# Performance work log

Hardware: AMD Instinct MI355X
Metric: run time of the kernel (lower is better)

## Reference

```python
import jax, jax.numpy as jnp
import numpy as np

B, S, DIN, D = 8, 1024, 512, 512


def _xavier(key, fan_in, fan_out):
    bound = float(np.sqrt(6.0 / (fan_in + fan_out)))
    return jax.random.uniform(key, (fan_in, fan_out), jnp.float32, -bound, bound)


def setup_inputs() -> dict:
    key = jax.random.key(0)
    ks = jax.random.split(key, 6)
    return {
        'x': jax.random.normal(ks[0], (B, S, DIN), jnp.float32),
        # weights stored as [in, out] (transpose of torch Linear.weight); biases zero-init per _init_weights
        'W_in': _xavier(ks[1], DIN, 4 * D), 'b_in': jnp.zeros((4 * D,), jnp.float32),
        'W_ig': _xavier(ks[2], D, D), 'b_ig': jnp.zeros((D,), jnp.float32),
        'W_fg': _xavier(ks[3], D, D), 'b_fg': jnp.zeros((D,), jnp.float32),
        'W_og': _xavier(ks[4], D, D), 'b_og': jnp.zeros((D,), jnp.float32),
        'W_out': _xavier(ks[5], D, D), 'b_out': jnp.zeros((D,), jnp.float32),
    }


def reference(x, W_in, b_in, W_ig, b_ig, W_fg, b_fg, W_og, b_og, W_out, b_out):
    b, s, _ = x.shape
    d = W_ig.shape[0]
    proj = x @ W_in + b_in                      # [B,S,4D]
    q, k, v, _g = jnp.split(proj, 4, axis=-1)   # g (silu branch) is unused in the original loop
    q = jnp.tanh(q)
    k = jnp.tanh(k)
    # dropout is identity in eval mode
    i_g = jax.nn.sigmoid(v @ W_ig + b_ig)       # per-step gates are pointwise linears -> batch them
    f_g = jax.nn.sigmoid(v @ W_fg + b_fg)
    o_g = jax.nn.sigmoid(v @ W_og + b_og)

    def step(carry, ts):
        C, n = carry                            # C: [B,D,D], n: [B,D]
        qt, kt, vt, it, ft, ot = ts             # each [B,D]
        C = ft[:, :, None] * C + it[:, :, None] * (kt[:, :, None] * vt[:, None, :])
        n = ft * n + it * kt
        h_cand = jnp.einsum('bd,bde->be', qt, C)
        denom = jnp.maximum(jnp.sum(qt * n, axis=-1, keepdims=True), 1e-6)
        h = ot * h_cand / denom
        return (C, n), h

    tm = lambda a: jnp.swapaxes(a, 0, 1)        # time-major for scan
    C0 = jnp.zeros((b, d, d), x.dtype)
    n0 = jnp.zeros((b, d), x.dtype)
    (Cf, nf), hs = jax.lax.scan(step, (C0, n0), (tm(q), tm(k), tm(v), tm(i_g), tm(f_g), tm(o_g)))
    hs = jnp.swapaxes(hs, 0, 1)                 # [B,S,D]
    out = hs @ W_out + b_out
    return out, Cf, nf, hs[:, -1, :]
```

## Files before the change

kernel.cpp:

```cpp
#include <hip/hip_runtime.h>

#define S_ 1024
#define D_ 512
#define DCH 4
#define NDCH 256
#define CT 32
#define NCT 32

using bf16x8 = __attribute__((ext_vector_type(8))) short;
using f32x4  = __attribute__((ext_vector_type(4))) float;

__device__ __forceinline__ unsigned short f2bf(float x) {
    unsigned int u = __float_as_uint(x);
    u = (u + 0x7FFFu + ((u >> 16) & 1u)) >> 16;
    return (unsigned short)u;
}
__device__ __forceinline__ float bf2f(unsigned short s) {
    return __uint_as_float(((unsigned int)s) << 16);
}
__device__ __forceinline__ bf16x8 cvt8(const float* __restrict__ p) {
    float4 a = *(const float4*)p;
    float4 b = *(const float4*)(p + 4);
    bf16x8 r;
    r[0] = (short)f2bf(a.x); r[1] = (short)f2bf(a.y);
    r[2] = (short)f2bf(a.z); r[3] = (short)f2bf(a.w);
    r[4] = (short)f2bf(b.x); r[5] = (short)f2bf(b.y);
    r[6] = (short)f2bf(b.z); r[7] = (short)f2bf(b.w);
    return r;
}
__device__ __forceinline__ void gload_lds16(const void* g, void* l) {
    __builtin_amdgcn_global_load_lds(
        (const __attribute__((address_space(1))) void*)g,
        (__attribute__((address_space(3))) void*)l, 16, 0, 0);
}


__global__ __launch_bounds__(256)
void prep_w(const float* __restrict__ W_in, const float* __restrict__ W_ig,
            const float* __restrict__ W_fg, const float* __restrict__ W_og,
            const float* __restrict__ W_out,
            unsigned short* __restrict__ Wh, unsigned short* __restrict__ Wl)
{
    const int n    = blockIdx.x * 256 + threadIdx.x;
    const int kblk = blockIdx.y;

    const float* src; int ldw, col;
    if (n < 1536)       { src = W_in;  ldw = 2048; col = n; }
    else if (n < 3072)  {
        const int g = (n - 1536) >> 9;
        src = (g == 0) ? W_ig : (g == 1) ? W_fg : W_og;
        ldw = 512; col = (n - 1536) & 511;
    } else              { src = W_out; ldw = 512; col = n - 3072; }

    unsigned int hw[16], lw[16];
#pragma unroll
    for (int j = 0; j < 32; j += 2) {
        const int k = kblk * 32 + j;
        float f0 = src[(size_t)k * ldw + col];
        float f1 = src[(size_t)(k + 1) * ldw + col];
        unsigned short h0 = f2bf(f0), h1 = f2bf(f1);
        unsigned short l0 = f2bf(f0 - bf2f(h0)), l1 = f2bf(f1 - bf2f(h1));
        hw[j >> 1] = (unsigned int)h0 | ((unsigned int)h1 << 16);
        lw[j >> 1] = (unsigned int)l0 | ((unsigned int)l1 << 16);
    }
    const size_t base = ((size_t)(n >> 7) * 16 + kblk) * 4096 + ((n & 127) << 5);
    const int perm = (n >> 1) & 3;
#pragma unroll
    for (int g = 0; g < 4; ++g) {
        const size_t dst = base + (size_t)((g ^ perm) << 3);
        *(uint4*)(Wh + dst) = make_uint4(hw[g*4], hw[g*4+1], hw[g*4+2], hw[g*4+3]);
        *(uint4*)(Wl + dst) = make_uint4(lw[g*4], lw[g*4+1], lw[g*4+2], lw[g*4+3]);
    }
}

__global__ __launch_bounds__(256)
void cvt_a(const float* __restrict__ A, int lda,
           unsigned short* __restrict__ Ah, unsigned short* __restrict__ Al)
{
    const int m    = blockIdx.x * 256 + threadIdx.x;
    const int kblk = blockIdx.y;
    const float* p = A + (size_t)m * lda + kblk * 32;
    const size_t base = ((size_t)(m >> 7) * 16 + kblk) * 4096 + ((m & 127) << 5);
    const int perm = (m >> 1) & 3;
#pragma unroll
    for (int g = 0; g < 4; ++g) {
        float4 a = *(const float4*)(p + g * 8);
        float4 b = *(const float4*)(p + g * 8 + 4);
        float f[8] = {a.x, a.y, a.z, a.w, b.x, b.y, b.z, b.w};
        unsigned int hw[4], lw[4];
#pragma unroll
        for (int j = 0; j < 4; ++j) {
            unsigned short h0 = f2bf(f[2*j]), h1 = f2bf(f[2*j+1]);
            unsigned short l0 = f2bf(f[2*j] - bf2f(h0));
            unsigned short l1 = f2bf(f[2*j+1] - bf2f(h1));
            hw[j] = (unsigned int)h0 | ((unsigned int)h1 << 16);
            lw[j] = (unsigned int)l0 | ((unsigned int)l1 << 16);
        }
        const size_t dst = base + (size_t)((g ^ perm) << 3);
        *(uint4*)(Ah + dst) = make_uint4(hw[0], hw[1], hw[2], hw[3]);
        *(uint4*)(Al + dst) = make_uint4(lw[0], lw[1], lw[2], lw[3]);
    }
}

template<int MODE>
__global__ __launch_bounds__(256)
void gemm_mfma(const unsigned short* __restrict__ Ah,
               const unsigned short* __restrict__ Al,
               const unsigned short* __restrict__ Wh,
               const unsigned short* __restrict__ Wl,
               const float* __restrict__ qkv,
               const float* __restrict__ bb0, const float* __restrict__ bb1,
               const float* __restrict__ bb2,
               float* __restrict__ Co, int ldc,
               unsigned short* __restrict__ Av, unsigned short* __restrict__ Alv)
{
    __shared__ unsigned short lds[2][4][4096];

    const int tid  = threadIdx.x;
    const int lane = tid & 63;
    const int wv   = tid >> 6;
    const int nbt  = (MODE == 2) ? 4 : 12;
    const int cpx  = gridDim.x >> 3;
    const int swz  = (blockIdx.x & 7) * cpx + (blockIdx.x >> 3);
    const int n0blk = swz % nbt;
    const int m0blk = swz / nbt;
    const int l15  = lane & 15;
    const int kg   = lane >> 4;
    const int nbase = (MODE == 0) ? 0 : (MODE == 1) ? 1536 : 3072;

    const size_t abase = (size_t)m0blk * 16 * 4096;
    const size_t wbase = (size_t)((nbase >> 7) + n0blk) * 16 * 4096;

    f32x4 acc[4][4];
#pragma unroll
    for (int mf = 0; mf < 4; ++mf)
#pragma unroll
        for (int nf = 0; nf < 4; ++nf) acc[mf][nf] = (f32x4){0.f, 0.f, 0.f, 0.f};

    auto STAGE = [&](int buf, int kblk) {
        const unsigned short* srcs[4] = {
            Ah + abase + (size_t)kblk * 4096, Al + abase + (size_t)kblk * 4096,
            Wh + wbase + (size_t)kblk * 4096, Wl + wbase + (size_t)kblk * 4096};
#pragma unroll
        for (int p = 0; p < 4; ++p)
#pragma unroll
            for (int h = 0; h < 2; ++h)
                gload_lds16(srcs[p] + h * 2048 + (size_t)tid * 8,
                            &lds[buf][p][h * 2048 + wv * 512]);
    };

    STAGE(0, 0);
    __syncthreads();

    int cur = 0;
    for (int ks = 0; ks < 16; ++ks) {
        if (ks + 1 < 16) STAGE(cur ^ 1, ks + 1);

        bf16x8 ah[4], al[4], bh[4], bl[4];
#pragma unroll
        for (int i = 0; i < 4; ++i) {
            const int ra = (wv >> 1) * 64 + i * 16 + l15;
            const int oa = ra * 32 + ((kg ^ ((ra >> 1) & 3)) << 3);
            ah[i] = *(const bf16x8*)&lds[cur][0][oa];
            al[i] = *(const bf16x8*)&lds[cur][1][oa];
            const int rw = (wv & 1) * 64 + i * 16 + l15;
            const int ow = rw * 32 + ((kg ^ ((rw >> 1) & 3)) << 3);
            bh[i] = *(const bf16x8*)&lds[cur][2][ow];
            bl[i] = *(const bf16x8*)&lds[cur][3][ow];
        }
#pragma unroll
        for (int nf = 0; nf < 4; ++nf)
#pragma unroll
            for (int mf = 0; mf < 4; ++mf) {
                acc[mf][nf] = __builtin_amdgcn_mfma_f32_16x16x32_bf16(ah[mf], bh[nf], acc[mf][nf], 0, 0, 0);
                acc[mf][nf] = __builtin_amdgcn_mfma_f32_16x16x32_bf16(al[mf], bh[nf], acc[mf][nf], 0, 0, 0);
                acc[mf][nf] = __builtin_amdgcn_mfma_f32_16x16x32_bf16(ah[mf], bl[nf], acc[mf][nf], 0, 0, 0);
            }
        __syncthreads();
        cur ^= 1;
    }

    const int m0 = m0blk * 128 + (wv >> 1) * 64;
    const int n0 = n0blk * 128 + (wv & 1) * 64;
#pragma unroll
    for (int mf = 0; mf < 4; ++mf) {
#pragma unroll
        for (int vi = 0; vi < 4; ++vi) {
            const int m = m0 + mf * 16 + kg * 4 + vi;
            float* crow = Co + (size_t)m * ldc;
#pragma unroll
            for (int nf = 0; nf < 4; ++nf) {
                const int n = n0 + nf * 16 + l15;
                float bias;
                if (MODE == 1) {
                    const int g = n >> 9;
                    bias = (g == 0 ? bb0 : g == 1 ? bb1 : bb2)[n & 511];
                } else {
                    bias = bb0[n];
                }
                float v = acc[mf][nf][vi] + bias;
                if (MODE == 0) {
                    if (n < 1024) v = tanhf(v);
                } else if (MODE == 1) {
                    v = 1.0f / (1.0f + expf(-v));
                    if (n < 512) v *= qkv[(size_t)m * 1536 + 512 + n];
                }
                crow[n] = v;
                if (MODE == 0 && Av != nullptr && n >= 1024) {
                    const int k = n - 1024;
                    unsigned short h0 = f2bf(v);
                    unsigned short l0 = f2bf(v - bf2f(h0));
                    const size_t dst = ((size_t)(m >> 7) * 16 + (k >> 5)) * 4096
                                     + ((m & 127) << 5)
                                     + ((((k >> 3) & 3) ^ ((m >> 1) & 3)) << 3)
                                     + (k & 7);
                    Av[dst]  = h0;
                    Alv[dst] = l0;
                }
            }
        }
    }
}

__global__ __launch_bounds__(512)
void nscan_local(const float* __restrict__ GG,
                 double* __restrict__ nend, double* __restrict__ Dend)
{
    const int b = blockIdx.x >> 8;
    const int c = blockIdx.x & 255;
    const int d = threadIdx.x;
    const float* gb = GG + (size_t)b * S_ * 1536 + (size_t)c * DCH * 1536;
    double n = 0.0, P = 1.0;
    for (int u = 0; u < DCH; ++u) {
        const float* row = gb + (size_t)u * 1536;
        const double ik = (double)row[d];
        const double f  = (double)row[512 + d];
        n = fma(f, n, ik);
        P *= f;
    }
    nend[(size_t)blockIdx.x * 512 + d] = n;
    Dend[(size_t)blockIdx.x * 512 + d] = P;
}

__global__ __launch_bounds__(512)
void nscan_stitch(const double* __restrict__ nend, const double* __restrict__ Dend,
                  double* __restrict__ n0a, float* __restrict__ nfO)
{
    const int b = blockIdx.x;
    const int d = threadIdx.x;
    double n0 = 0.0;
    for (int c = 0; c < NDCH; ++c) {
        const size_t idx = ((size_t)(b * NDCH + c)) * 512 + d;
        n0a[idx] = n0;
        n0 = fma(Dend[idx], n0, nend[idx]);
    }
    nfO[(size_t)b * 512 + d] = (float)n0;
}

__global__ __launch_bounds__(256)
void denom_kernel(const float* __restrict__ QKV, const float* __restrict__ GG,
                  const double* __restrict__ n0a, float* __restrict__ invd)
{
    const int lane = threadIdx.x & 63;
    const int widx = blockIdx.x * 4 + (threadIdx.x >> 6);
    const int b    = widx >> 8;
    const int c    = widx & 255;
    const int d0   = 4 * lane;

    const float* qb = QKV + (size_t)b * S_ * 1536 + (size_t)c * DCH * 1536;
    const float* gb = GG  + (size_t)b * S_ * 1536 + (size_t)c * DCH * 1536;
    const double* sp = n0a + (size_t)widx * 512;

    double n[2][4];
#pragma unroll
    for (int r = 0; r < 2; ++r) {
        double2 a = *(const double2*)(sp + d0 + 256 * r);
        double2 bb = *(const double2*)(sp + d0 + 256 * r + 2);
        n[r][0] = a.x; n[r][1] = a.y; n[r][2] = bb.x; n[r][3] = bb.y;
    }

    for (int t0 = 0; t0 < DCH; t0 += 4) {
        double dq[4];
#pragma unroll
        for (int i = 0; i < 4; ++i) {
            const float* qr = qb + (size_t)(t0 + i) * 1536;
            const float* gr = gb + (size_t)(t0 + i) * 1536;
            double acc = 0.0;
#pragma unroll
            for (int r = 0; r < 2; ++r) {
                float4 qf = *(const float4*)(qr + d0 + 256 * r);
                float4 kf = *(const float4*)(gr + d0 + 256 * r);
                float4 ff = *(const float4*)(gr + 512 + d0 + 256 * r);
                const float* qp = (const float*)&qf;
                const float* kp = (const float*)&kf;
                const float* fp = (const float*)&ff;
#pragma unroll
                for (int j = 0; j < 4; ++j) {
                    n[r][j] = fma((double)fp[j], n[r][j], (double)kp[j]);
                    acc = fma((double)qp[j], n[r][j], acc);
                }
            }
            dq[i] = acc;
        }
        double u0 = dq[0] + __shfl_xor(dq[0], 32);
        double u1 = dq[1] + __shfl_xor(dq[1], 32);
        double u2 = dq[2] + __shfl_xor(dq[2], 32);
        double u3 = dq[3] + __shfl_xor(dq[3], 32);
        double w0 = (lane & 32) ? u2 : u0;
        double w1 = (lane & 32) ? u3 : u1;
        w0 += __shfl_xor(w0, 16);
        w1 += __shfl_xor(w1, 16);
        double y = (lane & 16) ? w1 : w0;
        y += __shfl_xor(y, 8); y += __shfl_xor(y, 4);
        y += __shfl_xor(y, 2); y += __shfl_xor(y, 1);
        if ((lane & 15) == 0) {
            const int g = lane >> 4;
            const double den = (y > 1e-6) ? y : 1e-6;
            invd[(size_t)b * S_ + c * DCH + t0 + g] = (float)(1.0 / den);
        }
    }
}

__global__ __launch_bounds__(512)
void chunk_prep(float* __restrict__ qkv, float* __restrict__ gg)
{
    const int b = blockIdx.x >> 5;
    const int c = blockIdx.x & 31;
    const int d = threadIdx.x;
    float* qr = qkv + ((size_t)(b * S_ + c * CT)) * 1536 + d;
    float* gr = gg  + ((size_t)(b * S_ + c * CT)) * 1536 + d;
    float* ft = gr + 512;
    float F = 1.f;
    for (int u = 0; u < CT; ++u) {
        const float q = qr[0], ik = gr[0], f = gr[512];
        F *= f;
        qr[0] = q * F;
        gr[0] = ik / F;
        qr += 1536; gr += 1536;
    }
    ft[0] = F;
}

__global__ __launch_bounds__(256)
void chunk_A(const float* __restrict__ qkv, const float* __restrict__ gg,
             float* __restrict__ h1out)
{
    const int b   = blockIdx.x >> 5;
    const int c   = blockIdx.x & 31;
    const int tid = threadIdx.x;
    const int t   = tid & 31;
    const int g   = tid >> 5;

    __shared__ float sA[32][33];

    const size_t rb = (size_t)(b * S_ + c * CT);
    const float* qr = qkv + (rb + t) * 1536;
    const float* kb = gg + rb * 1536;

    {
        const int s0 = g * 4;
        const float* k0 = kb + (size_t)(s0 + 0) * 1536;
        const float* k1 = kb + (size_t)(s0 + 1) * 1536;
        const float* k2 = kb + (size_t)(s0 + 2) * 1536;
        const float* k3 = kb + (size_t)(s0 + 3) * 1536;
        float a0 = 0.f, a1 = 0.f, a2 = 0.f, a3 = 0.f;
        for (int d4 = 0; d4 < 512; d4 += 4) {
            float4 qv = *(const float4*)(qr + d4);
            float4 x0 = *(const float4*)(k0 + d4);
            float4 x1 = *(const float4*)(k1 + d4);
            float4 x2 = *(const float4*)(k2 + d4);
            float4 x3 = *(const float4*)(k3 + d4);
            a0 = fmaf(qv.x, x0.x, a0); a0 = fmaf(qv.y, x0.y, a0);
            a0 = fmaf(qv.z, x0.z, a0); a0 = fmaf(qv.w, x0.w, a0);
            a1 = fmaf(qv.x, x1.x, a1); a1 = fmaf(qv.y, x1.y, a1);
            a1 = fmaf(qv.z, x1.z, a1); a1 = fmaf(qv.w, x1.w, a1);
            a2 = fmaf(qv.x, x2.x, a2); a2 = fmaf(qv.y, x2.y, a2);
            a2 = fmaf(qv.z, x2.z, a2); a2 = fmaf(qv.w, x2.w, a2);
            a3 = fmaf(qv.x, x3.x, a3); a3 = fmaf(qv.y, x3.y, a3);
            a3 = fmaf(qv.z, x3.z, a3); a3 = fmaf(qv.w, x3.w, a3);
        }
        sA[t][s0 + 0] = (s0 + 0 <= t) ? a0 : 0.f;
        sA[t][s0 + 1] = (s0 + 1 <= t) ? a1 : 0.f;
        sA[t][s0 + 2] = (s0 + 2 <= t) ? a2 : 0.f;
        sA[t][s0 + 3] = (s0 + 3 <= t) ? a3 : 0.f;
    }
    __syncthreads();

    {
        const int e0 = g * 64;
        float4 h[16];
#pragma unroll
        for (int m = 0; m < 16; ++m) h[m] = make_float4(0.f, 0.f, 0.f, 0.f);
        const float* vb = qkv + rb * 1536 + 1024 + e0;
        for (int s = 0; s < CT; ++s) {
            const float a = sA[t][s];
            const float* vr = vb + (size_t)s * 1536;
#pragma unroll
            for (int m = 0; m < 16; ++m) {
                float4 vv = *(const float4*)(vr + m * 4);
                h[m].x = fmaf(a, vv.x, h[m].x);
                h[m].y = fmaf(a, vv.y, h[m].y);
                h[m].z = fmaf(a, vv.z, h[m].z);
                h[m].w = fmaf(a, vv.w, h[m].w);
            }
        }
        float* orow = h1out + (rb + t) * 512 + e0;
#pragma unroll
        for (int m = 0; m < 16; ++m) *(float4*)(orow + m * 4) = h[m];
    }
}

__global__ __launch_bounds__(1024)
void chunk_cacc(const float* __restrict__ qkv, const float* __restrict__ gg,
                unsigned short* __restrict__ snap, int c0)
{
    __shared__ unsigned short vT[256][40];
    __shared__ unsigned short kT[512][40];

    const int b    = blockIdx.x;
    const int lc   = blockIdx.y;
    const int eh   = blockIdx.z;
    const int c    = c0 + lc;
    const int tid  = threadIdx.x;
    const int lane = tid & 63;
    const int wv   = tid >> 6;
    const int l15  = lane & 15;
    const int kg   = lane >> 4;

    const size_t rb = (size_t)(b * S_ + c * CT);
    const size_t sb = ((size_t)lc * 8 + b) * 512;

    if (tid < 256) {
        const float* vp = qkv + rb * 1536 + 1024 + eh * 256 + tid;
        unsigned int pk[16];
#pragma unroll
        for (int u = 0; u < 32; u += 2) {
            float f0 = vp[(size_t)u * 1536];
            float f1 = vp[(size_t)(u + 1) * 1536];
            pk[u >> 1] = (unsigned int)f2bf(f0) | ((unsigned int)f2bf(f1) << 16);
        }
        uint4* dst = (uint4*)&vT[tid][0];
        dst[0] = make_uint4(pk[0],  pk[1],  pk[2],  pk[3]);
        dst[1] = make_uint4(pk[4],  pk[5],  pk[6],  pk[7]);
        dst[2] = make_uint4(pk[8],  pk[9],  pk[10], pk[11]);
        dst[3] = make_uint4(pk[12], pk[13], pk[14], pk[15]);
    } else if (tid < 768) {
        const int d = tid - 256;
        const float* kp = gg + rb * 1536 + d;
        unsigned int pk[16];
#pragma unroll
        for (int u = 0; u < 32; u += 2) {
            float f0 = kp[(size_t)u * 1536];
            float f1 = kp[(size_t)(u + 1) * 1536];
            pk[u >> 1] = (unsigned int)f2bf(f0) | ((unsigned int)f2bf(f1) << 16);
        }
        uint4* dst = (uint4*)&kT[d][0];
        dst[0] = make_uint4(pk[0],  pk[1],  pk[2],  pk[3]);
        dst[1] = make_uint4(pk[4],  pk[5],  pk[6],  pk[7]);
        dst[2] = make_uint4(pk[8],  pk[9],  pk[10], pk[11]);
        dst[3] = make_uint4(pk[12], pk[13], pk[14], pk[15]);
    }
    __syncthreads();

    const int ebase = (wv & 3) * 64;
    const int dbase = (wv >> 2) * 128;

    bf16x8 a[4];
#pragma unroll
    for (int me = 0; me < 4; ++me)
        a[me] = *(const bf16x8*)&vT[ebase + me * 16 + l15][kg * 8];

#pragma unroll
    for (int dp = 0; dp < 2; ++dp) {
        f32x4 acc[4][4];
#pragma unroll
        for (int me = 0; me < 4; ++me)
#pragma unroll
            for (int nd = 0; nd < 4; ++nd) acc[me][nd] = (f32x4){0.f, 0.f, 0.f, 0.f};

#pragma unroll
        for (int nd = 0; nd < 4; ++nd) {
            bf16x8 bfr = *(const bf16x8*)&kT[dbase + dp * 64 + nd * 16 + l15][kg * 8];
#pragma unroll
            for (int me = 0; me < 4; ++me)
                acc[me][nd] = __builtin_amdgcn_mfma_f32_16x16x32_bf16(a[me], bfr, acc[me][nd], 0, 0, 0);
        }

#pragma unroll
        for (int me = 0; me < 4; ++me)
#pragma unroll
            for (int vi = 0; vi < 4; ++vi) {
                const int e = eh * 256 + ebase + me * 16 + kg * 4 + vi;
                unsigned short* row = snap + (sb + e) * 512 + dbase + dp * 64;
#pragma unroll
                for (int nd = 0; nd < 4; ++nd)
                    row[nd * 16 + l15] = f2bf(acc[me][nd][vi]);
            }
    }
}

__global__ __launch_bounds__(256)
void chunk_cscan(const float* __restrict__ gg,
                 unsigned short* __restrict__ snap, float* __restrict__ Cst,
                 float* __restrict__ CfO, int c0, int nc)
{
    const int tid  = threadIdx.x;
    const int lane = tid & 63;
    const int wv   = tid >> 6;
    const int b    = blockIdx.x;
    const int eg   = blockIdx.y;
    const int dh   = blockIdx.z;
    const int ew   = eg * 16 + wv * 4;
    const int d0   = dh * 256 + 4 * lane;

    const float* gb = gg + (size_t)b * S_ * 1536;

    float C[4][4];
    if (c0 == 0) {
#pragma unroll
        for (int i = 0; i < 4; ++i)
#pragma unroll
            for (int j = 0; j < 4; ++j) C[i][j] = 0.f;
    } else {
#pragma unroll
        for (int j = 0; j < 4; ++j) {
            float4 cv = *(const float4*)&Cst[((size_t)b * 512 + d0 + j) * 512 + ew];
            C[0][j] = cv.x; C[1][j] = cv.y; C[2][j] = cv.z; C[3][j] = cv.w;
        }
    }

    ushort4 A0[4]; float4 F0;
    {
        const size_t sb = ((size_t)0 * 8 + b) * 512;
#pragma unroll
        for (int i = 0; i < 4; ++i)
            A0[i] = *(const ushort4*)(snap + (sb + ew + i) * 512 + d0);
        F0 = *(const float4*)(gb + (size_t)(c0 * CT) * 1536 + 512 + d0);
    }

    for (int lc = 0; lc < nc; ++lc) {
        ushort4 A1[4]; float4 F1;
        if (lc + 1 < nc) {
            const size_t sb = ((size_t)(lc + 1) * 8 + b) * 512;
#pragma unroll
            for (int i = 0; i < 4; ++i)
                A1[i] = *(const ushort4*)(snap + (sb + ew + i) * 512 + d0);
            F1 = *(const float4*)(gb + (size_t)((c0 + lc + 1) * CT) * 1536 + 512 + d0);
        }

        const int c = c0 + lc;
        if (c > 0) {
            const size_t sb = ((size_t)lc * 8 + b) * 512;
#pragma unroll
            for (int i = 0; i < 4; ++i) {
                uint2 pk;
                pk.x = (unsigned int)f2bf(C[i][0]) | ((unsigned int)f2bf(C[i][1]) << 16);
                pk.y = (unsigned int)f2bf(C[i][2]) | ((unsigned int)f2bf(C[i][3]) << 16);
                *(uint2*)(snap + (sb + ew + i) * 512 + d0) = pk;
            }
        }

        const float* fp = (const float*)&F0;
#pragma unroll
        for (int i = 0; i < 4; ++i) {
            C[i][0] = fp[0] * (C[i][0] + bf2f(A0[i].x));
            C[i][1] = fp[1] * (C[i][1] + bf2f(A0[i].y));
            C[i][2] = fp[2] * (C[i][2] + bf2f(A0[i].z));
            C[i][3] = fp[3] * (C[i][3] + bf2f(A0[i].w));
        }

        if (lc + 1 < nc) {
#pragma unroll
            for (int i = 0; i < 4; ++i) A0[i] = A1[i];
            F0 = F1;
        }
    }

    float* outp = (c0 + nc == NCT) ? CfO : Cst;
#pragma unroll
    for (int j = 0; j < 4; ++j)
        *(float4*)&outp[((size_t)b * 512 + d0 + j) * 512 + ew] =
            make_float4(C[0][j], C[1][j], C[2][j], C[3][j]);
}

__global__ __launch_bounds__(256)
void chunk_h2(const float* __restrict__ qkv, const float* __restrict__ gg,
              const unsigned short* __restrict__ snap,
              const float* __restrict__ invd,
              float* __restrict__ hs, float* __restrict__ hlO, int c0)
{
    const int eh   = blockIdx.x;
    const int lc   = blockIdx.y;
    const int b    = blockIdx.z;
    const int c    = c0 + lc;
    const int tid  = threadIdx.x;
    const int lane = tid & 63;
    const int wv   = tid >> 6;
    const int n0   = eh * 256 + wv * 64;
    const int l15  = lane & 15;
    const int kg   = lane >> 4;

    const size_t rb = (size_t)(b * S_ + c * CT);

    f32x4 acc[2][4];
#pragma unroll
    for (int mf = 0; mf < 2; ++mf)
#pragma unroll
        for (int nf = 0; nf < 4; ++nf) acc[mf][nf] = (f32x4){0.f, 0.f, 0.f, 0.f};

    if (c > 0) {
        const unsigned short* cb = snap + ((size_t)(lc * 8 + b) * 512) * 512;
        const float* q0p = qkv + (rb + l15) * 1536;
        const float* q1p = qkv + (rb + 16 + l15) * 1536;
#pragma unroll 4
        for (int k0 = 0; k0 < 512; k0 += 32) {
            const int kb = k0 + kg * 8;
            bf16x8 a0 = cvt8(q0p + kb);
            bf16x8 a1 = cvt8(q1p + kb);
#pragma unroll
            for (int nf = 0; nf < 4; ++nf) {
                const unsigned short* bp = cb + (size_t)(n0 + nf * 16 + l15) * 512 + kb;
                bf16x8 bf = *(const bf16x8*)bp;
                acc[0][nf] = __builtin_amdgcn_mfma_f32_16x16x32_bf16(a0, bf, acc[0][nf], 0, 0, 0);
                acc[1][nf] = __builtin_amdgcn_mfma_f32_16x16x32_bf16(a1, bf, acc[1][nf], 0, 0, 0);
            }
        }
    }

    const float* ivp = invd + (size_t)b * S_ + c * CT;
#pragma unroll
    for (int mf = 0; mf < 2; ++mf) {
#pragma unroll
        for (int vi = 0; vi < 4; ++vi) {
            const int tl  = mf * 16 + kg * 4 + vi;
            const float ivt = ivp[tl];
            float* hrow       = hs + (rb + tl) * 512;
            const float* orow = gg + (rb + tl) * 1536 + 1024;
            const bool last = (c * CT + tl == S_ - 1);
#pragma unroll
            for (int nf = 0; nf < 4; ++nf) {
                const int e  = n0 + nf * 16 + l15;
                const float h1 = hrow[e];
                const float ov = orow[e];
                const float r  = (acc[mf][nf][vi] + h1) * ov * ivt;
                hrow[e] = r;
                if (last) hlO[(size_t)b * 512 + e] = r;
            }
        }
    }
}

extern "C" void kernel_launch(void* const* d_in, const int* in_sizes, int n_in,
                              void* d_out, int out_size, void* d_ws, size_t ws_size,
                              hipStream_t stream)
{
    const float* x    = (const float*)d_in[0];
    const float* W_in = (const float*)d_in[1];
    const float* b_in = (const float*)d_in[2];
    const float* W_ig = (const float*)d_in[3];
    const float* b_ig = (const float*)d_in[4];
    const float* W_fg = (const float*)d_in[5];
    const float* b_fg = (const float*)d_in[6];
    const float* W_og = (const float*)d_in[7];
    const float* b_og = (const float*)d_in[8];
    const float* W_out= (const float*)d_in[9];
    const float* b_out= (const float*)d_in[10];

    float* out   = (float*)d_out;
    float* CfO   = out + (size_t)8 * 1024 * 512;
    float* nfO   = CfO + (size_t)8 * 512 * 512;
    float* hlO   = nfO + (size_t)8 * 512;

    float* qkv = (float*)d_ws;
    float* gg  = qkv + (size_t)8192 * 1536;
    float* hsb = gg  + (size_t)8192 * 1536;
    double* nend = (double*)hsb;
    double* Dend = nend + (size_t)8 * NDCH * 512;
    double* n0a  = Dend + (size_t)8 * NDCH * 512;
    float*  invd = hsb + (size_t)8192 * 512;
    float*  Cst  = invd + 8192;
    unsigned short* Wh = (unsigned short*)(Cst + (size_t)8 * 512 * 512);
    unsigned short* Wl = Wh + (size_t)3584 * 512;
    unsigned short* snap = Wl + (size_t)3584 * 512;

    const size_t WSB   = (size_t)((char*)snap - (char*)d_ws);
    const size_t SNAPC = (size_t)8 * 512 * 512 * 2;
    const size_t SLOTS = (size_t)8 * 512 * 512;
    int nc; unsigned short* Ah;
    if (ws_size >= WSB + 32 * SNAPC)      { nc = 32; Ah = snap; }
    else if (ws_size >= WSB + 8 * SNAPC)  { nc = 8;  Ah = snap; }
    else                                  { nc = 2;  Ah = snap + 2 * (SNAPC / 2); }
    unsigned short* Al = Ah + (size_t)8192 * 512;

    unsigned short* Av  = nullptr;
    unsigned short* Alv = nullptr;
    if (nc >= 8) { Av = snap + 4 * SLOTS; Alv = Av + (size_t)8192 * 512; }

    prep_w<<<dim3(14, 16), 256, 0, stream>>>(W_in, W_ig, W_fg, W_og, W_out, Wh, Wl);
    cvt_a<<<dim3(32, 16), 256, 0, stream>>>(x, 512, Ah, Al);
    gemm_mfma<0><<<768, 256, 0, stream>>>(
        Ah, Al, Wh, Wl, qkv, b_in, b_in, b_in, qkv, 1536, Av, Alv);
    const unsigned short* Aga = Av  ? Av  : Ah;
    const unsigned short* Agl = Alv ? Alv : Al;
    if (!Av) cvt_a<<<dim3(32, 16), 256, 0, stream>>>(qkv + 1024, 1536, Ah, Al);
    gemm_mfma<1><<<768, 256, 0, stream>>>(
        Aga, Agl, Wh, Wl, qkv, b_ig, b_fg, b_og, gg, 1536, nullptr, nullptr);
    nscan_local <<<2048, 512, 0, stream>>>(gg, nend, Dend);
    nscan_stitch<<<   8, 512, 0, stream>>>(nend, Dend, n0a, nfO);
    denom_kernel<<< 512, 256, 0, stream>>>(qkv, gg, n0a, invd);
    chunk_prep<<<256, 512, 0, stream>>>(qkv, gg);
    chunk_A<<<256, 256, 0, stream>>>(qkv, gg, hsb);
    for (int c0 = 0; c0 < NCT; c0 += nc) {
        chunk_cacc <<<dim3(8, nc, 2), 1024, 0, stream>>>(qkv, gg, snap, c0);
        chunk_cscan<<<dim3(8, 32, 2), 256, 0, stream>>>(gg, snap, Cst, CfO, c0, nc);
        chunk_h2   <<<dim3(2, nc, 8), 256, 0, stream>>>(qkv, gg, snap, invd, hsb, hlO, c0);
    }
    cvt_a<<<dim3(32, 16), 256, 0, stream>>>(hsb, 512, Ah, Al);
    gemm_mfma<2><<<256, 256, 0, stream>>>(
        Ah, Al, Wh, Wl, qkv, b_out, b_out, b_out, out, 512, nullptr, nullptr);
}
```

Measured before the change: 433.0 us.

## Move intra-chunk attention to split-bf16 MFMA and double n-scan chunk length

chunk_A now computes the 32x32 Q·K^T chunk scores and the scores·V product with bf16 MFMA. Each fp32 operand is split into hi and lo bf16 parts and three MFMAs are accumulated to keep accuracy close to fp32. This replaces scalar fp32 FMA loops. V is transposed into LDS in two 256-column halves. Separately, the n-scan chunk length grows from 4 to 8, halving the block counts of nscan_local and denom_kernel, which leaves more sequential work per thread.

```diff
diff --git a/kernel.cpp b/kernel.cpp
--- a/kernel.cpp
+++ b/kernel.cpp
@@ -2,8 +2,8 @@
 
 #define S_ 1024
 #define D_ 512
-#define DCH 4
-#define NDCH 256
+#define DCH 8
+#define NDCH 128
 #define CT 32
 #define NCT 32
 
@@ -27,6 +27,18 @@
     r[4] = (short)f2bf(b.x); r[5] = (short)f2bf(b.y);
     r[6] = (short)f2bf(b.z); r[7] = (short)f2bf(b.w);
     return r;
+}
+__device__ __forceinline__ void cvt8pair(const float* __restrict__ p,
+                                         bf16x8& hi, bf16x8& lo) {
+    float4 a = *(const float4*)p;
+    float4 b = *(const float4*)(p + 4);
+    float f[8] = {a.x, a.y, a.z, a.w, b.x, b.y, b.z, b.w};
+#pragma unroll
+    for (int j = 0; j < 8; ++j) {
+        unsigned short h = f2bf(f[j]);
+        hi[j] = (short)h;
+        lo[j] = (short)f2bf(f[j] - bf2f(h));
+    }
 }
 __device__ __forceinline__ void gload_lds16(const void* g, void* l) {
     __builtin_amdgcn_global_load_lds(
@@ -226,8 +238,8 @@
 void nscan_local(const float* __restrict__ GG,
                  double* __restrict__ nend, double* __restrict__ Dend)
 {
-    const int b = blockIdx.x >> 8;
-    const int c = blockIdx.x & 255;
+    const int b = blockIdx.x >> 7;
+    const int c = blockIdx.x & 127;
     const int d = threadIdx.x;
     const float* gb = GG + (size_t)b * S_ * 1536 + (size_t)c * DCH * 1536;
     double n = 0.0, P = 1.0;
@@ -263,8 +275,8 @@
 {
     const int lane = threadIdx.x & 63;
     const int widx = blockIdx.x * 4 + (threadIdx.x >> 6);
-    const int b    = widx >> 8;
-    const int c    = widx & 255;
+    const int b    = widx >> 7;
+    const int c    = widx & 127;
     const int d0   = 4 * lane;
 
     const float* qb = QKV + (size_t)b * S_ * 1536 + (size_t)c * DCH * 1536;
@@ -345,68 +357,111 @@
 void chunk_A(const float* __restrict__ qkv, const float* __restrict__ gg,
              float* __restrict__ h1out)
 {
-    const int b   = blockIdx.x >> 5;
-    const int c   = blockIdx.x & 31;
-    const int tid = threadIdx.x;
-    const int t   = tid & 31;
-    const int g   = tid >> 5;
-
-    __shared__ float sA[32][33];
+    __shared__ float sA[32][36];
+    __shared__ unsigned short vTh[256][40];
+    __shared__ unsigned short vTl[256][40];
+
+    const int b    = blockIdx.x >> 5;
+    const int c    = blockIdx.x & 31;
+    const int tid  = threadIdx.x;
+    const int lane = tid & 63;
+    const int wv   = tid >> 6;
+    const int l15  = lane & 15;
+    const int kg   = lane >> 4;
 
     const size_t rb = (size_t)(b * S_ + c * CT);
-    const float* qr = qkv + (rb + t) * 1536;
-    const float* kb = gg + rb * 1536;
-
+
+    const int qi = wv >> 1, qj = wv & 1;
     {
-        const int s0 = g * 4;
-        const float* k0 = kb + (size_t)(s0 + 0) * 1536;
-        const float* k1 = kb + (size_t)(s0 + 1) * 1536;
-        const float* k2 = kb + (size_t)(s0 + 2) * 1536;
-        const float* k3 = kb + (size_t)(s0 + 3) * 1536;
-        float a0 = 0.f, a1 = 0.f, a2 = 0.f, a3 = 0.f;
-        for (int d4 = 0; d4 < 512; d4 += 4) {
-            float4 qv = *(const float4*)(qr + d4);
-            float4 x0 = *(const float4*)(k0 + d4);
-            float4 x1 = *(const float4*)(k1 + d4);
-            float4 x2 = *(const float4*)(k2 + d4);
-            float4 x3 = *(const float4*)(k3 + d4);
-            a0 = fmaf(qv.x, x0.x, a0); a0 = fmaf(qv.y, x0.y, a0);
-            a0 = fmaf(qv.z, x0.z, a0); a0 = fmaf(qv.w, x0.w, a0);
-            a1 = fmaf(qv.x, x1.x, a1); a1 = fmaf(qv.y, x1.y, a1);
-            a1 = fmaf(qv.z, x1.z, a1); a1 = fmaf(qv.w, x1.w, a1);
-            a2 = fmaf(qv.x, x2.x, a2); a2 = fmaf(qv.y, x2.y, a2);
-            a2 = fmaf(qv.z, x2.z, a2); a2 = fmaf(qv.w, x2.w, a2);
-            a3 = fmaf(qv.x, x3.x, a3); a3 = fmaf(qv.y, x3.y, a3);
-            a3 = fmaf(qv.z, x3.z, a3); a3 = fmaf(qv.w, x3.w, a3);
-        }
-        sA[t][s0 + 0] = (s0 + 0 <= t) ? a0 : 0.f;
-        sA[t][s0 + 1] = (s0 + 1 <= t) ? a1 : 0.f;
-        sA[t][s0 + 2] = (s0 + 2 <= t) ? a2 : 0.f;
-        sA[t][s0 + 3] = (s0 + 3 <= t) ? a3 : 0.f;
-    }
-    __syncthreads();
-
-    {
-        const int e0 = g * 64;
-        float4 h[16];
-#pragma unroll
-        for (int m = 0; m < 16; ++m) h[m] = make_float4(0.f, 0.f, 0.f, 0.f);
-        const float* vb = qkv + rb * 1536 + 1024 + e0;
-        for (int s = 0; s < CT; ++s) {
-            const float a = sA[t][s];
-            const float* vr = vb + (size_t)s * 1536;
-#pragma unroll
-            for (int m = 0; m < 16; ++m) {
-                float4 vv = *(const float4*)(vr + m * 4);
-                h[m].x = fmaf(a, vv.x, h[m].x);
-                h[m].y = fmaf(a, vv.y, h[m].y);
-                h[m].z = fmaf(a, vv.z, h[m].z);
-                h[m].w = fmaf(a, vv.w, h[m].w);
-            }
-        }
-        float* orow = h1out + (rb + t) * 512 + e0;
-#pragma unroll
-        for (int m = 0; m < 16; ++m) *(float4*)(orow + m * 4) = h[m];
+        const float* qrow = qkv + (rb + qi * 16 + l15) * 1536;
+        const float* krow = gg  + (rb + qj * 16 + l15) * 1536;
+        f32x4 accA = (f32x4){0.f, 0.f, 0.f, 0.f};
+#pragma unroll 4
+        for (int ks = 0; ks < 16; ++ks) {
+            const int kb = ks * 32 + kg * 8;
+            bf16x8 ah, al, bh, bl;
+            cvt8pair(qrow + kb, ah, al);
+            cvt8pair(krow + kb, bh, bl);
+            accA = __builtin_amdgcn_mfma_f32_16x16x32_bf16(ah, bh, accA, 0, 0, 0);
+            accA = __builtin_amdgcn_mfma_f32_16x16x32_bf16(al, bh, accA, 0, 0, 0);
+            accA = __builtin_amdgcn_mfma_f32_16x16x32_bf16(ah, bl, accA, 0, 0, 0);
+        }
+#pragma unroll
+        for (int vi = 0; vi < 4; ++vi) {
+            const int t = qi * 16 + kg * 4 + vi;
+            const int s = qj * 16 + l15;
+            sA[t][s] = (s <= t) ? accA[vi] : 0.f;
+        }
+    }
+
+    for (int half = 0; half < 2; ++half) {
+        {
+            const float* vp = qkv + rb * 1536 + 1024 + half * 256 + tid;
+            unsigned int ph[16], pl[16];
+#pragma unroll
+            for (int u = 0; u < 32; u += 2) {
+                float f0 = vp[(size_t)u * 1536];
+                float f1 = vp[(size_t)(u + 1) * 1536];
+                unsigned short h0 = f2bf(f0), h1 = f2bf(f1);
+                unsigned short l0 = f2bf(f0 - bf2f(h0)), l1 = f2bf(f1 - bf2f(h1));
+                ph[u >> 1] = (unsigned int)h0 | ((unsigned int)h1 << 16);
+                pl[u >> 1] = (unsigned int)l0 | ((unsigned int)l1 << 16);
+            }
+            if (half == 1) __syncthreads();
+            uint4* dh = (uint4*)&vTh[tid][0];
+            dh[0] = make_uint4(ph[0],  ph[1],  ph[2],  ph[3]);
+            dh[1] = make_uint4(ph[4],  ph[5],  ph[6],  ph[7]);
+            dh[2] = make_uint4(ph[8],  ph[9],  ph[10], ph[11]);
+            dh[3] = make_uint4(ph[12], ph[13], ph[14], ph[15]);
+            uint4* dl = (uint4*)&vTl[tid][0];
+            dl[0] = make_uint4(pl[0],  pl[1],  pl[2],  pl[3]);
+            dl[1] = make_uint4(pl[4],  pl[5],  pl[6],  pl[7]);
+            dl[2] = make_uint4(pl[8],  pl[9],  pl[10], pl[11]);
+            dl[3] = make_uint4(pl[12], pl[13], pl[14], pl[15]);
+        }
+        __syncthreads();
+
+        bf16x8 afh[2], afl[2];
+#pragma unroll
+        for (int mf = 0; mf < 2; ++mf) {
+            const float* ar = &sA[mf * 16 + l15][kg * 8];
+#pragma unroll
+            for (int j = 0; j < 8; ++j) {
+                unsigned short h = f2bf(ar[j]);
+                afh[mf][j] = (short)h;
+                afl[mf][j] = (short)f2bf(ar[j] - bf2f(h));
+            }
+        }
+
+        const int ebL = wv * 64;
+        f32x4 acc[2][4];
+#pragma unroll
+        for (int mf = 0; mf < 2; ++mf)
+#pragma unroll
+            for (int nf = 0; nf < 4; ++nf) acc[mf][nf] = (f32x4){0.f, 0.f, 0.f, 0.f};
+
+#pragma unroll
+        for (int nf = 0; nf < 4; ++nf) {
+            bf16x8 bh = *(const bf16x8*)&vTh[ebL + nf * 16 + l15][kg * 8];
+            bf16x8 bl = *(const bf16x8*)&vTl[ebL + nf * 16 + l15][kg * 8];
+#pragma unroll
+            for (int mf = 0; mf < 2; ++mf) {
+                acc[mf][nf] = __builtin_amdgcn_mfma_f32_16x16x32_bf16(afh[mf], bh, acc[mf][nf], 0, 0, 0);
+                acc[mf][nf] = __builtin_amdgcn_mfma_f32_16x16x32_bf16(afl[mf], bh, acc[mf][nf], 0, 0, 0);
+                acc[mf][nf] = __builtin_amdgcn_mfma_f32_16x16x32_bf16(afh[mf], bl, acc[mf][nf], 0, 0, 0);
+            }
+        }
+
+#pragma unroll
+        for (int mf = 0; mf < 2; ++mf)
+#pragma unroll
+            for (int vi = 0; vi < 4; ++vi) {
+                const int t = mf * 16 + kg * 4 + vi;
+                float* hrow = h1out + (rb + t) * 512 + half * 256 + ebL;
+#pragma unroll
+                for (int nf = 0; nf < 4; ++nf)
+                    hrow[nf * 16 + l15] = acc[mf][nf][vi];
+            }
     }
 }
 
@@ -705,9 +760,9 @@
     if (!Av) cvt_a<<<dim3(32, 16), 256, 0, stream>>>(qkv + 1024, 1536, Ah, Al);
     gemm_mfma<1><<<768, 256, 0, stream>>>(
         Aga, Agl, Wh, Wl, qkv, b_ig, b_fg, b_og, gg, 1536, nullptr, nullptr);
-    nscan_local <<<2048, 512, 0, stream>>>(gg, nend, Dend);
+    nscan_local <<<1024, 512, 0, stream>>>(gg, nend, Dend);
     nscan_stitch<<<   8, 512, 0, stream>>>(nend, Dend, n0a, nfO);
-    denom_kernel<<< 512, 256, 0, stream>>>(qkv, gg, n0a, invd);
+    denom_kernel<<< 256, 256, 0, stream>>>(qkv, gg, n0a, invd);
     chunk_prep<<<256, 512, 0, stream>>>(qkv, gg);
     chunk_A<<<256, 256, 0, stream>>>(qkv, gg, hsb);
     for (int c0 = 0; c0 < NCT; c0 += nc) {
```

Result: faster. 375.4 us (-13.3%).
